# Kernel optimization log

Measured on AMD Instinct MI355X. Metric: run time of the kernel, lower is better.

## Reference

```python
import jax, jax.numpy as jnp
import numpy as np
import math

IN_CH = 256
OUT_CH = 256
N_JOINTS = 25
BATCH = 16384


def setup_inputs() -> dict:
    key = jax.random.key(0)
    kx, kw = jax.random.split(key)
    x = jax.random.normal(kx, (N_JOINTS, BATCH, IN_CH), dtype=jnp.float32)
    stdv = 1.0 / math.sqrt(OUT_CH)
    weight = jax.random.uniform(kw, (IN_CH, OUT_CH), dtype=jnp.float32,
                                minval=-stdv, maxval=stdv)
    return {"x": x, "weight": weight}


def reference(x, weight):
    # x: (N, B, D) -> attention over joints N per batch element
    xb = jnp.transpose(x, (1, 0, 2))            # (B, N, D)
    s3 = jnp.einsum('bnd,bmd->bnm', xb, xb)     # (B, N, N) self-similarity
    s = jax.nn.softmax(s3, axis=-1)
    out = jnp.einsum('bnm,bmd->bnd', s, xb)     # (B, N, D)
    out = out @ weight                           # (B, N, out_channels)
    return out
```

## Files before the change

### kernel.cpp

```cpp
#include <hip/hip_runtime.h>

#define GRID   1024
#define BLOCK  256
#define BATCH  16384
#define NJ     25
#define DEPTH  256
#define ITERS  (BATCH / GRID)

typedef short s16x8 __attribute__((ext_vector_type(8)));
typedef short s16x4 __attribute__((ext_vector_type(4)));
typedef float f32x4 __attribute__((ext_vector_type(4)));

__device__ __forceinline__ short f2bf(float f) {
  union { float f; unsigned u; } c; c.f = f;
  unsigned r = (c.u + 0x7FFFu + ((c.u >> 16) & 1u)) >> 16;
  return (short)r;
}

#define MFMA(a, b, c) __builtin_amdgcn_mfma_f32_16x16x32_bf16((a), (b), (c), 0, 0, 0)

__global__ __launch_bounds__(BLOCK, 2)
void geo_gcn_fused(const float* __restrict__ x,
                   const float* __restrict__ w,
                   float* __restrict__ out)
{
  __shared__ short As[2][32][72];
  __shared__ short Ps[32][40];
  __shared__ float S3[32][33];
  __shared__ short Yt[4][64][40];

  const int tid  = threadIdx.x;
  const int wv   = tid >> 6;
  const int lane = tid & 63;
  const int quad = lane >> 4;
  const int l16  = lane & 15;

  s16x8 wf[8][4];
  {
    const int ncol = wv * 64 + l16;
#pragma unroll
    for (int ks = 0; ks < 8; ++ks)
#pragma unroll
      for (int td = 0; td < 4; ++td) {
        const float* wp = w + (size_t)(ks * 32 + quad * 8) * DEPTH + ncol + td * 16;
#pragma unroll
        for (int j = 0; j < 8; ++j)
          wf[ks][td][j] = f2bf(wp[(size_t)j * DEPTH]);
      }
  }

  const int tm_s = wv >> 1;
  const int tn_s = wv & 1;

  const int srow = tid >> 3;
  const int sq   = tid & 7;

  for (int ib = 0; ib < ITERS; ++ib) {
    const int b = blockIdx.x + GRID * ib;

    f32x4 sacc = (f32x4){0.f, 0.f, 0.f, 0.f};
    f32x4 yacc[2][4];
#pragma unroll
    for (int i = 0; i < 2; ++i)
#pragma unroll
      for (int j = 0; j < 4; ++j) yacc[i][j] = (f32x4){0.f, 0.f, 0.f, 0.f};

    const float* xb = x + ((size_t)srow * BATCH + b) * DEPTH + sq * 8;

    {
      float4 c0, c1;
      if (srow < NJ) {
        c0 = *(const float4*)(xb + 0);
        c1 = *(const float4*)(xb + 4);
      } else { c0 = make_float4(0.f, 0.f, 0.f, 0.f); c1 = c0; }
      s16x8 h;
      h[0]=f2bf(c0.x); h[1]=f2bf(c0.y); h[2]=f2bf(c0.z); h[3]=f2bf(c0.w);
      h[4]=f2bf(c1.x); h[5]=f2bf(c1.y); h[6]=f2bf(c1.z); h[7]=f2bf(c1.w);
      *(s16x8*)&As[0][srow][sq * 8] = h;
    }
    __syncthreads();

#pragma unroll
    for (int kc = 0; kc < 4; ++kc) {
      float4 n0, n1;
      if (kc < 3) {
        if (srow < NJ) {
          n0 = *(const float4*)(xb + (kc + 1) * 64);
          n1 = *(const float4*)(xb + (kc + 1) * 64 + 4);
        } else { n0 = make_float4(0.f, 0.f, 0.f, 0.f); n1 = n0; }
      }
      const int buf = kc & 1;
#pragma unroll
      for (int s = 0; s < 2; ++s) {
        s16x8 a0 = *(const s16x8*)&As[buf][l16][s * 32 + quad * 8];
        s16x8 a1 = *(const s16x8*)&As[buf][16 + l16][s * 32 + quad * 8];
        sacc = MFMA(tm_s ? a1 : a0, tn_s ? a1 : a0, sacc);
        const int ks = kc * 2 + s;
#pragma unroll
        for (int td = 0; td < 4; ++td) {
          yacc[0][td] = MFMA(a0, wf[ks][td], yacc[0][td]);
          yacc[1][td] = MFMA(a1, wf[ks][td], yacc[1][td]);
        }
      }
      if (kc < 3) {
        s16x8 h;
        h[0]=f2bf(n0.x); h[1]=f2bf(n0.y); h[2]=f2bf(n0.z); h[3]=f2bf(n0.w);
        h[4]=f2bf(n1.x); h[5]=f2bf(n1.y); h[6]=f2bf(n1.z); h[7]=f2bf(n1.w);
        *(s16x8*)&As[1 - buf][srow][sq * 8] = h;
      }
      __syncthreads();
    }

#pragma unroll
    for (int r = 0; r < 4; ++r)
      S3[tm_s * 16 + quad * 4 + r][tn_s * 16 + l16] = sacc[r];
    __syncthreads();

    if (tid < 32) {
      const int row = tid;
      float mx = -3.0e38f;
      for (int j = 0; j < NJ; ++j) mx = fmaxf(mx, S3[row][j]);
      float sum = 0.f;
      for (int j = 0; j < NJ; ++j) sum += __expf(S3[row][j] - mx);
      const float rinv = 1.0f / sum;
      for (int j = 0; j < NJ; ++j) Ps[row][j] = f2bf(__expf(S3[row][j] - mx) * rinv);
      for (int j = NJ; j < 32; ++j) Ps[row][j] = 0;
    }
    __syncthreads();

#pragma unroll
    for (int tm = 0; tm < 2; ++tm)
#pragma unroll
      for (int td = 0; td < 4; ++td) {
        s16x4 hy;
#pragma unroll
        for (int r = 0; r < 4; ++r) hy[r] = f2bf(yacc[tm][td][r]);
        *(s16x4*)&Yt[wv][td * 16 + l16][tm * 16 + quad * 4] = hy;
      }

    s16x8 pf0 = *(const s16x8*)&Ps[l16][quad * 8];
    s16x8 pf1 = *(const s16x8*)&Ps[16 + l16][quad * 8];
    const f32x4 zero4 = (f32x4){0.f, 0.f, 0.f, 0.f};
    float* ob = out + (size_t)b * NJ * DEPTH + wv * 64 + l16;
#pragma unroll
    for (int td = 0; td < 4; ++td) {
      s16x8 yb = *(const s16x8*)&Yt[wv][td * 16 + l16][quad * 8];
      f32x4 o0 = MFMA(pf0, yb, zero4);
      f32x4 o1 = MFMA(pf1, yb, zero4);
#pragma unroll
      for (int r = 0; r < 4; ++r) {
        const int n0 = quad * 4 + r;
        ob[(size_t)n0 * DEPTH + td * 16] = o0[r];
        const int n1 = 16 + quad * 4 + r;
        if (n1 < NJ) ob[(size_t)n1 * DEPTH + td * 16] = o1[r];
      }
    }
  }
}

extern "C" void kernel_launch(void* const* d_in, const int* in_sizes, int n_in,
                              void* d_out, int out_size, void* d_ws, size_t ws_size,
                              hipStream_t stream) {
  (void)in_sizes; (void)n_in; (void)out_size; (void)d_ws; (void)ws_size;
  const float* x = (const float*)d_in[0];
  const float* w = (const float*)d_in[1];
  float* out = (float*)d_out;
  geo_gcn_fused<<<dim3(GRID), dim3(BLOCK), 0, stream>>>(x, w, out);
}
```

Before: 727.2 us.

## Use 8-wave blocks with whole-sample double-buffered prefetch and parallel softmax

Doubles the block to 512 threads (8 waves) and halves the grid. Each wave now owns 32 output columns, so it keeps half as many weight fragments in registers. Each block stages a full 25x256 bf16 sample in LDS and prefetches the next sample during the current iteration, which replaces the per-k-chunk loop and its repeated barriers. Softmax is spread over 256 threads using shuffle reductions instead of 32 serial threads. The tradeoffs are larger LDS use, only 4 of the 8 waves computing S, and prefetch registers that stay live across the whole iteration.

```diff
diff --git a/kernel.cpp b/kernel.cpp
--- a/kernel.cpp
+++ b/kernel.cpp
@@ -1,7 +1,7 @@
 #include <hip/hip_runtime.h>
 
-#define GRID   1024
-#define BLOCK  256
+#define GRID   512
+#define BLOCK  512
 #define BATCH  16384
 #define NJ     25
 #define DEPTH  256
@@ -19,15 +19,15 @@
 
 #define MFMA(a, b, c) __builtin_amdgcn_mfma_f32_16x16x32_bf16((a), (b), (c), 0, 0, 0)
 
-__global__ __launch_bounds__(BLOCK, 2)
+__global__ __launch_bounds__(BLOCK, 4)
 void geo_gcn_fused(const float* __restrict__ x,
                    const float* __restrict__ w,
                    float* __restrict__ out)
 {
-  __shared__ short As[2][32][72];
+  __shared__ short As[2][32][264];
   __shared__ short Ps[32][40];
   __shared__ float S3[32][33];
-  __shared__ short Yt[4][64][40];
+  __shared__ short Yt[8][32][40];
 
   const int tid  = threadIdx.x;
   const int wv   = tid >> 6;
@@ -35,13 +35,13 @@
   const int quad = lane >> 4;
   const int l16  = lane & 15;
 
-  s16x8 wf[8][4];
+  s16x8 wf[8][2];
   {
-    const int ncol = wv * 64 + l16;
+    const int ncol = wv * 32 + l16;
 #pragma unroll
     for (int ks = 0; ks < 8; ++ks)
 #pragma unroll
-      for (int td = 0; td < 4; ++td) {
+      for (int td = 0; td < 2; ++td) {
         const float* wp = w + (size_t)(ks * 32 + quad * 8) * DEPTH + ncol + td * 16;
 #pragma unroll
         for (int j = 0; j < 8; ++j)
@@ -49,89 +49,99 @@
       }
   }
 
-  const int tm_s = wv >> 1;
+  const int srow = tid >> 4;
+  const int sc   = tid & 15;
+  const int tm_s = (wv >> 1) & 1;
   const int tn_s = wv & 1;
 
-  const int srow = tid >> 3;
-  const int sq   = tid & 7;
+  const float* xrow = x + (size_t)srow * BATCH * DEPTH + sc * 16;
+
+  {
+    float4 c0 = make_float4(0.f, 0.f, 0.f, 0.f), c1 = c0, c2 = c0, c3 = c0;
+    if (srow < NJ) {
+      const float* xp = xrow + (size_t)blockIdx.x * DEPTH;
+      c0 = *(const float4*)(xp + 0);  c1 = *(const float4*)(xp + 4);
+      c2 = *(const float4*)(xp + 8);  c3 = *(const float4*)(xp + 12);
+    }
+    s16x8 h0, h1;
+    h0[0]=f2bf(c0.x); h0[1]=f2bf(c0.y); h0[2]=f2bf(c0.z); h0[3]=f2bf(c0.w);
+    h0[4]=f2bf(c1.x); h0[5]=f2bf(c1.y); h0[6]=f2bf(c1.z); h0[7]=f2bf(c1.w);
+    h1[0]=f2bf(c2.x); h1[1]=f2bf(c2.y); h1[2]=f2bf(c2.z); h1[3]=f2bf(c2.w);
+    h1[4]=f2bf(c3.x); h1[5]=f2bf(c3.y); h1[6]=f2bf(c3.z); h1[7]=f2bf(c3.w);
+    *(s16x8*)&As[0][srow][sc * 16]     = h0;
+    *(s16x8*)&As[0][srow][sc * 16 + 8] = h1;
+  }
+  __syncthreads();
 
   for (int ib = 0; ib < ITERS; ++ib) {
-    const int b = blockIdx.x + GRID * ib;
+    const int b   = blockIdx.x + GRID * ib;
+    const int buf = ib & 1;
+
+    float4 n0 = make_float4(0.f, 0.f, 0.f, 0.f), n1 = n0, n2 = n0, n3 = n0;
+    if ((ib + 1 < ITERS) && (srow < NJ)) {
+      const float* xp = xrow + (size_t)(b + GRID) * DEPTH;
+      n0 = *(const float4*)(xp + 0);  n1 = *(const float4*)(xp + 4);
+      n2 = *(const float4*)(xp + 8);  n3 = *(const float4*)(xp + 12);
+    }
 
     f32x4 sacc = (f32x4){0.f, 0.f, 0.f, 0.f};
-    f32x4 yacc[2][4];
+    f32x4 yacc[2][2];
 #pragma unroll
     for (int i = 0; i < 2; ++i)
 #pragma unroll
-      for (int j = 0; j < 4; ++j) yacc[i][j] = (f32x4){0.f, 0.f, 0.f, 0.f};
+      for (int j = 0; j < 2; ++j) yacc[i][j] = (f32x4){0.f, 0.f, 0.f, 0.f};
 
-    const float* xb = x + ((size_t)srow * BATCH + b) * DEPTH + sq * 8;
+#pragma unroll
+    for (int ks = 0; ks < 8; ++ks) {
+      s16x8 a0 = *(const s16x8*)&As[buf][l16][ks * 32 + quad * 8];
+      s16x8 a1 = *(const s16x8*)&As[buf][16 + l16][ks * 32 + quad * 8];
+      if (wv < 4) sacc = MFMA(tm_s ? a1 : a0, tn_s ? a1 : a0, sacc);
+      yacc[0][0] = MFMA(a0, wf[ks][0], yacc[0][0]);
+      yacc[0][1] = MFMA(a0, wf[ks][1], yacc[0][1]);
+      yacc[1][0] = MFMA(a1, wf[ks][0], yacc[1][0]);
+      yacc[1][1] = MFMA(a1, wf[ks][1], yacc[1][1]);
+    }
 
-    {
-      float4 c0, c1;
-      if (srow < NJ) {
-        c0 = *(const float4*)(xb + 0);
-        c1 = *(const float4*)(xb + 4);
-      } else { c0 = make_float4(0.f, 0.f, 0.f, 0.f); c1 = c0; }
-      s16x8 h;
-      h[0]=f2bf(c0.x); h[1]=f2bf(c0.y); h[2]=f2bf(c0.z); h[3]=f2bf(c0.w);
-      h[4]=f2bf(c1.x); h[5]=f2bf(c1.y); h[6]=f2bf(c1.z); h[7]=f2bf(c1.w);
-      *(s16x8*)&As[0][srow][sq * 8] = h;
+    if (wv < 4) {
+#pragma unroll
+      for (int r = 0; r < 4; ++r)
+        S3[tm_s * 16 + quad * 4 + r][tn_s * 16 + l16] = sacc[r];
     }
     __syncthreads();
 
+    if (tid < 256) {
+      const int row = tid >> 3, c8 = tid & 7;
+      float v[4]; float mx = -3.0e38f;
 #pragma unroll
-    for (int kc = 0; kc < 4; ++kc) {
-      float4 n0, n1;
-      if (kc < 3) {
-        if (srow < NJ) {
-          n0 = *(const float4*)(xb + (kc + 1) * 64);
-          n1 = *(const float4*)(xb + (kc + 1) * 64 + 4);
-        } else { n0 = make_float4(0.f, 0.f, 0.f, 0.f); n1 = n0; }
+      for (int i = 0; i < 4; ++i) {
+        const int j = c8 + 8 * i;
+        v[i] = (j < NJ) ? S3[row][j] : -3.0e38f;
+        mx = fmaxf(mx, v[i]);
       }
-      const int buf = kc & 1;
+      mx = fmaxf(mx, __shfl_xor(mx, 1));
+      mx = fmaxf(mx, __shfl_xor(mx, 2));
+      mx = fmaxf(mx, __shfl_xor(mx, 4));
+      float e[4]; float sum = 0.f;
 #pragma unroll
-      for (int s = 0; s < 2; ++s) {
-        s16x8 a0 = *(const s16x8*)&As[buf][l16][s * 32 + quad * 8];
-        s16x8 a1 = *(const s16x8*)&As[buf][16 + l16][s * 32 + quad * 8];
-        sacc = MFMA(tm_s ? a1 : a0, tn_s ? a1 : a0, sacc);
-        const int ks = kc * 2 + s;
+      for (int i = 0; i < 4; ++i) {
+        const int j = c8 + 8 * i;
+        e[i] = (j < NJ) ? __expf(v[i] - mx) : 0.f;
+        sum += e[i];
+      }
+      sum += __shfl_xor(sum, 1);
+      sum += __shfl_xor(sum, 2);
+      sum += __shfl_xor(sum, 4);
+      const float rinv = 1.0f / sum;
 #pragma unroll
-        for (int td = 0; td < 4; ++td) {
-          yacc[0][td] = MFMA(a0, wf[ks][td], yacc[0][td]);
-          yacc[1][td] = MFMA(a1, wf[ks][td], yacc[1][td]);
-        }
-      }
-      if (kc < 3) {
-        s16x8 h;
-        h[0]=f2bf(n0.x); h[1]=f2bf(n0.y); h[2]=f2bf(n0.z); h[3]=f2bf(n0.w);
-        h[4]=f2bf(n1.x); h[5]=f2bf(n1.y); h[6]=f2bf(n1.z); h[7]=f2bf(n1.w);
-        *(s16x8*)&As[1 - buf][srow][sq * 8] = h;
-      }
-      __syncthreads();
-    }
-
-#pragma unroll
-    for (int r = 0; r < 4; ++r)
-      S3[tm_s * 16 + quad * 4 + r][tn_s * 16 + l16] = sacc[r];
-    __syncthreads();
-
-    if (tid < 32) {
-      const int row = tid;
-      float mx = -3.0e38f;
-      for (int j = 0; j < NJ; ++j) mx = fmaxf(mx, S3[row][j]);
-      float sum = 0.f;
-      for (int j = 0; j < NJ; ++j) sum += __expf(S3[row][j] - mx);
-      const float rinv = 1.0f / sum;
-      for (int j = 0; j < NJ; ++j) Ps[row][j] = f2bf(__expf(S3[row][j] - mx) * rinv);
-      for (int j = NJ; j < 32; ++j) Ps[row][j] = 0;
+      for (int i = 0; i < 4; ++i)
+        Ps[row][c8 + 8 * i] = f2bf(e[i] * rinv);
     }
     __syncthreads();
 
 #pragma unroll
     for (int tm = 0; tm < 2; ++tm)
 #pragma unroll
-      for (int td = 0; td < 4; ++td) {
+      for (int td = 0; td < 2; ++td) {
         s16x4 hy;
 #pragma unroll
         for (int r = 0; r < 4; ++r) hy[r] = f2bf(yacc[tm][td][r]);
@@ -140,21 +150,31 @@
 
     s16x8 pf0 = *(const s16x8*)&Ps[l16][quad * 8];
     s16x8 pf1 = *(const s16x8*)&Ps[16 + l16][quad * 8];
-    const f32x4 zero4 = (f32x4){0.f, 0.f, 0.f, 0.f};
-    float* ob = out + (size_t)b * NJ * DEPTH + wv * 64 + l16;
+    const f32x4 z4 = (f32x4){0.f, 0.f, 0.f, 0.f};
+    float* ob = out + (size_t)b * NJ * DEPTH + wv * 32 + l16;
 #pragma unroll
-    for (int td = 0; td < 4; ++td) {
+    for (int td = 0; td < 2; ++td) {
       s16x8 yb = *(const s16x8*)&Yt[wv][td * 16 + l16][quad * 8];
-      f32x4 o0 = MFMA(pf0, yb, zero4);
-      f32x4 o1 = MFMA(pf1, yb, zero4);
+      f32x4 o0 = MFMA(pf0, yb, z4);
+      f32x4 o1 = MFMA(pf1, yb, z4);
 #pragma unroll
       for (int r = 0; r < 4; ++r) {
-        const int n0 = quad * 4 + r;
-        ob[(size_t)n0 * DEPTH + td * 16] = o0[r];
-        const int n1 = 16 + quad * 4 + r;
-        if (n1 < NJ) ob[(size_t)n1 * DEPTH + td * 16] = o1[r];
+        ob[(size_t)(quad * 4 + r) * DEPTH + td * 16] = o0[r];
+        const int nr = 16 + quad * 4 + r;
+        if (nr < NJ) ob[(size_t)nr * DEPTH + td * 16] = o1[r];
       }
     }
+
+    if (ib + 1 < ITERS) {
+      s16x8 h0, h1;
+      h0[0]=f2bf(n0.x); h0[1]=f2bf(n0.y); h0[2]=f2bf(n0.z); h0[3]=f2bf(n0.w);
+      h0[4]=f2bf(n1.x); h0[5]=f2bf(n1.y); h0[6]=f2bf(n1.z); h0[7]=f2bf(n1.w);
+      h1[0]=f2bf(n2.x); h1[1]=f2bf(n2.y); h1[2]=f2bf(n2.z); h1[3]=f2bf(n2.w);
+      h1[4]=f2bf(n3.x); h1[5]=f2bf(n3.y); h1[6]=f2bf(n3.z); h1[7]=f2bf(n3.w);
+      *(s16x8*)&As[1 - buf][srow][sc * 16]     = h0;
+      *(s16x8*)&As[1 - buf][srow][sc * 16 + 8] = h1;
+    }
+    __syncthreads();
   }
 }
 
```

New measurement: 793.5 us. +9.1%, slower.

## Assign one batch element per wavefront with register-resident softmax and LDS weights

Applied to the files above, without the earlier changes.

Each wavefront now processes a whole batch element on its own: it keeps the bf16 x fragments in registers, computes the 25x25 similarity with four MFMAs, and does the softmax with cross-lane shuffles. This removes the block-wide __syncthreads and the LDS staging for S3, Ps and Yt. The weight matrix moves from per-thread registers into a transposed bf16 LDS tile shared by 8 waves per block, and Y is repacked into MFMA operand layout with shuffles. The trade-off is about 132KB of LDS per block, which caps occupancy, and heavier register use from holding 16 x fragments per lane.

```diff
diff --git a/kernel.cpp b/kernel.cpp
--- a/kernel.cpp
+++ b/kernel.cpp
@@ -1,20 +1,25 @@
 #include <hip/hip_runtime.h>
 
-#define GRID   1024
-#define BLOCK  256
+#define GRID   256
+#define BLOCK  512
 #define BATCH  16384
 #define NJ     25
 #define DEPTH  256
-#define ITERS  (BATCH / GRID)
+#define WPB    8
+#define TOTW   (GRID * WPB)
+#define ELEMS  (BATCH / TOTW)
 
 typedef short s16x8 __attribute__((ext_vector_type(8)));
-typedef short s16x4 __attribute__((ext_vector_type(4)));
 typedef float f32x4 __attribute__((ext_vector_type(4)));
 
 __device__ __forceinline__ short f2bf(float f) {
   union { float f; unsigned u; } c; c.f = f;
   unsigned r = (c.u + 0x7FFFu + ((c.u >> 16) & 1u)) >> 16;
   return (short)r;
+}
+__device__ __forceinline__ unsigned pk2(float lo, float hi) {
+  return ((unsigned)(unsigned short)f2bf(hi) << 16) |
+         (unsigned)(unsigned short)f2bf(lo);
 }
 
 #define MFMA(a, b, c) __builtin_amdgcn_mfma_f32_16x16x32_bf16((a), (b), (c), 0, 0, 0)
@@ -24,135 +29,151 @@
                    const float* __restrict__ w,
                    float* __restrict__ out)
 {
-  __shared__ short As[2][32][72];
-  __shared__ short Ps[32][40];
-  __shared__ float S3[32][33];
-  __shared__ short Yt[4][64][40];
+  __shared__ short Wt[DEPTH][264];
 
   const int tid  = threadIdx.x;
   const int wv   = tid >> 6;
   const int lane = tid & 63;
-  const int quad = lane >> 4;
+  const int q    = lane >> 4;
   const int l16  = lane & 15;
 
-  s16x8 wf[8][4];
-  {
-    const int ncol = wv * 64 + l16;
+  for (int it = 0; it < 32; ++it) {
+    const int idx4 = tid + BLOCK * it;
+    const int k    = idx4 >> 6;
+    const int n4   = (idx4 & 63) << 2;
+    float4 wq = *(const float4*)(w + (size_t)k * DEPTH + n4);
+    Wt[n4 + 0][k] = f2bf(wq.x);
+    Wt[n4 + 1][k] = f2bf(wq.y);
+    Wt[n4 + 2][k] = f2bf(wq.z);
+    Wt[n4 + 3][k] = f2bf(wq.w);
+  }
+  __syncthreads();
+
+  const int gw = blockIdx.x * WPB + wv;
+  const float* xr0 = x + (size_t)l16 * BATCH * DEPTH + q * 8;
+  const float* xr1 = x + (size_t)(16 + l16) * BATCH * DEPTH + q * 8;
+  const bool  r1ok = (l16 < NJ - 16);
+  const int   sA   = ((q & 1) << 5) + l16;
+  const int   sB   = sA + 16;
+  const bool  lo32 = (lane < 32);
+  const f32x4 z4   = (f32x4){0.f, 0.f, 0.f, 0.f};
+  const s16x8 z8   = (s16x8){0, 0, 0, 0, 0, 0, 0, 0};
+
+  for (int i = 0; i < ELEMS; ++i) {
+    const int b = gw + TOTW * i;
+    const size_t boff = (size_t)b * DEPTH;
+
+    s16x8 af0[8], af1[8];
 #pragma unroll
-    for (int ks = 0; ks < 8; ++ks)
-#pragma unroll
-      for (int td = 0; td < 4; ++td) {
-        const float* wp = w + (size_t)(ks * 32 + quad * 8) * DEPTH + ncol + td * 16;
-#pragma unroll
-        for (int j = 0; j < 8; ++j)
-          wf[ks][td][j] = f2bf(wp[(size_t)j * DEPTH]);
-      }
-  }
-
-  const int tm_s = wv >> 1;
-  const int tn_s = wv & 1;
-
-  const int srow = tid >> 3;
-  const int sq   = tid & 7;
-
-  for (int ib = 0; ib < ITERS; ++ib) {
-    const int b = blockIdx.x + GRID * ib;
-
-    f32x4 sacc = (f32x4){0.f, 0.f, 0.f, 0.f};
-    f32x4 yacc[2][4];
-#pragma unroll
-    for (int i = 0; i < 2; ++i)
-#pragma unroll
-      for (int j = 0; j < 4; ++j) yacc[i][j] = (f32x4){0.f, 0.f, 0.f, 0.f};
-
-    const float* xb = x + ((size_t)srow * BATCH + b) * DEPTH + sq * 8;
-
-    {
-      float4 c0, c1;
-      if (srow < NJ) {
-        c0 = *(const float4*)(xb + 0);
-        c1 = *(const float4*)(xb + 4);
-      } else { c0 = make_float4(0.f, 0.f, 0.f, 0.f); c1 = c0; }
+    for (int ks = 0; ks < 8; ++ks) {
+      float4 c0 = *(const float4*)(xr0 + boff + ks * 32);
+      float4 c1 = *(const float4*)(xr0 + boff + ks * 32 + 4);
       s16x8 h;
       h[0]=f2bf(c0.x); h[1]=f2bf(c0.y); h[2]=f2bf(c0.z); h[3]=f2bf(c0.w);
       h[4]=f2bf(c1.x); h[5]=f2bf(c1.y); h[6]=f2bf(c1.z); h[7]=f2bf(c1.w);
-      *(s16x8*)&As[0][srow][sq * 8] = h;
+      af0[ks] = h;
+      s16x8 g = z8;
+      if (r1ok) {
+        float4 d0 = *(const float4*)(xr1 + boff + ks * 32);
+        float4 d1 = *(const float4*)(xr1 + boff + ks * 32 + 4);
+        g[0]=f2bf(d0.x); g[1]=f2bf(d0.y); g[2]=f2bf(d0.z); g[3]=f2bf(d0.w);
+        g[4]=f2bf(d1.x); g[5]=f2bf(d1.y); g[6]=f2bf(d1.z); g[7]=f2bf(d1.w);
+      }
+      af1[ks] = g;
     }
-    __syncthreads();
 
+    f32x4 s00 = z4, s01 = z4, s10 = z4, s11 = z4;
 #pragma unroll
-    for (int kc = 0; kc < 4; ++kc) {
-      float4 n0, n1;
-      if (kc < 3) {
-        if (srow < NJ) {
-          n0 = *(const float4*)(xb + (kc + 1) * 64);
-          n1 = *(const float4*)(xb + (kc + 1) * 64 + 4);
-        } else { n0 = make_float4(0.f, 0.f, 0.f, 0.f); n1 = n0; }
-      }
-      const int buf = kc & 1;
+    for (int ks = 0; ks < 8; ++ks) {
+      s00 = MFMA(af0[ks], af0[ks], s00);
+      s01 = MFMA(af0[ks], af1[ks], s01);
+      s10 = MFMA(af1[ks], af0[ks], s10);
+      s11 = MFMA(af1[ks], af1[ks], s11);
+    }
+
+    unsigned pd0[2][2], pd1[2][2];
+    {
+      float m0 = fmaxf(fmaxf(s00[0], s00[1]), fmaxf(s00[2], s00[3]));
+      float m1 = fmaxf(fmaxf(s01[0], s01[1]), fmaxf(s01[2], s01[3]));
 #pragma unroll
-      for (int s = 0; s < 2; ++s) {
-        s16x8 a0 = *(const s16x8*)&As[buf][l16][s * 32 + quad * 8];
-        s16x8 a1 = *(const s16x8*)&As[buf][16 + l16][s * 32 + quad * 8];
-        sacc = MFMA(tm_s ? a1 : a0, tn_s ? a1 : a0, sacc);
-        const int ks = kc * 2 + s;
-#pragma unroll
-        for (int td = 0; td < 4; ++td) {
-          yacc[0][td] = MFMA(a0, wf[ks][td], yacc[0][td]);
-          yacc[1][td] = MFMA(a1, wf[ks][td], yacc[1][td]);
+      for (int r = 0; r < 4; ++r) {
+        if (4 * q + r < 9) {
+          m0 = fmaxf(m0, s10[r]);
+          m1 = fmaxf(m1, s11[r]);
         }
       }
-      if (kc < 3) {
-        s16x8 h;
-        h[0]=f2bf(n0.x); h[1]=f2bf(n0.y); h[2]=f2bf(n0.z); h[3]=f2bf(n0.w);
-        h[4]=f2bf(n1.x); h[5]=f2bf(n1.y); h[6]=f2bf(n1.z); h[7]=f2bf(n1.w);
-        *(s16x8*)&As[1 - buf][srow][sq * 8] = h;
+      m0 = fmaxf(m0, __shfl_xor(m0, 16)); m0 = fmaxf(m0, __shfl_xor(m0, 32));
+      m1 = fmaxf(m1, __shfl_xor(m1, 16)); m1 = fmaxf(m1, __shfl_xor(m1, 32));
+      float e00[4], e01[4], e10[4], e11[4];
+      float t0 = 0.f, t1 = 0.f;
+#pragma unroll
+      for (int r = 0; r < 4; ++r) {
+        const bool v = (4 * q + r) < 9;
+        e00[r] = __expf(s00[r] - m0);
+        e10[r] = __expf(s01[r] - m1);
+        e01[r] = v ? __expf(s10[r] - m0) : 0.f;
+        e11[r] = v ? __expf(s11[r] - m1) : 0.f;
+        t0 += e00[r] + e01[r];
+        t1 += e10[r] + e11[r];
       }
-      __syncthreads();
+      t0 += __shfl_xor(t0, 16); t0 += __shfl_xor(t0, 32);
+      t1 += __shfl_xor(t1, 16); t1 += __shfl_xor(t1, 32);
+      const float i0 = 1.0f / t0, i1 = 1.0f / t1;
+      pd0[0][0] = pk2(e00[0] * i0, e00[1] * i0);
+      pd0[0][1] = pk2(e00[2] * i0, e00[3] * i0);
+      pd0[1][0] = pk2(e01[0] * i0, e01[1] * i0);
+      pd0[1][1] = pk2(e01[2] * i0, e01[3] * i0);
+      pd1[0][0] = pk2(e10[0] * i1, e10[1] * i1);
+      pd1[0][1] = pk2(e10[2] * i1, e10[3] * i1);
+      pd1[1][0] = pk2(e11[0] * i1, e11[1] * i1);
+      pd1[1][1] = pk2(e11[2] * i1, e11[3] * i1);
     }
 
+    s16x8 pf0, pf1;
+    {
+      union { unsigned u[4]; s16x8 v; } p0, p1;
+      int a, c;
+      a = __shfl((int)pd0[0][0], sA); c = __shfl((int)pd0[1][0], sA); p0.u[0] = lo32 ? a : c;
+      a = __shfl((int)pd0[0][1], sA); c = __shfl((int)pd0[1][1], sA); p0.u[1] = lo32 ? a : c;
+      a = __shfl((int)pd0[0][0], sB); c = __shfl((int)pd0[1][0], sB); p0.u[2] = lo32 ? a : c;
+      a = __shfl((int)pd0[0][1], sB); c = __shfl((int)pd0[1][1], sB); p0.u[3] = lo32 ? a : c;
+      a = __shfl((int)pd1[0][0], sA); c = __shfl((int)pd1[1][0], sA); p1.u[0] = lo32 ? a : c;
+      a = __shfl((int)pd1[0][1], sA); c = __shfl((int)pd1[1][1], sA); p1.u[1] = lo32 ? a : c;
+      a = __shfl((int)pd1[0][0], sB); c = __shfl((int)pd1[1][0], sB); p1.u[2] = lo32 ? a : c;
+      a = __shfl((int)pd1[0][1], sB); c = __shfl((int)pd1[1][1], sB); p1.u[3] = lo32 ? a : c;
+      pf0 = p0.v;
+      pf1 = p1.v;
+    }
+
+    float* ob = out + (size_t)b * NJ * DEPTH;
+#pragma unroll 2
+    for (int td = 0; td < 16; ++td) {
+      const short* wp = &Wt[16 * td + l16][q * 8];
+      f32x4 y0 = z4, y1 = z4;
 #pragma unroll
-    for (int r = 0; r < 4; ++r)
-      S3[tm_s * 16 + quad * 4 + r][tn_s * 16 + l16] = sacc[r];
-    __syncthreads();
-
-    if (tid < 32) {
-      const int row = tid;
-      float mx = -3.0e38f;
-      for (int j = 0; j < NJ; ++j) mx = fmaxf(mx, S3[row][j]);
-      float sum = 0.f;
-      for (int j = 0; j < NJ; ++j) sum += __expf(S3[row][j] - mx);
-      const float rinv = 1.0f / sum;
-      for (int j = 0; j < NJ; ++j) Ps[row][j] = f2bf(__expf(S3[row][j] - mx) * rinv);
-      for (int j = NJ; j < 32; ++j) Ps[row][j] = 0;
-    }
-    __syncthreads();
-
-#pragma unroll
-    for (int tm = 0; tm < 2; ++tm)
-#pragma unroll
-      for (int td = 0; td < 4; ++td) {
-        s16x4 hy;
-#pragma unroll
-        for (int r = 0; r < 4; ++r) hy[r] = f2bf(yacc[tm][td][r]);
-        *(s16x4*)&Yt[wv][td * 16 + l16][tm * 16 + quad * 4] = hy;
+      for (int ks = 0; ks < 8; ++ks) {
+        const s16x8 wb = *(const s16x8*)(wp + ks * 32);
+        y0 = MFMA(af0[ks], wb, y0);
+        y1 = MFMA(af1[ks], wb, y1);
       }
-
-    s16x8 pf0 = *(const s16x8*)&Ps[l16][quad * 8];
-    s16x8 pf1 = *(const s16x8*)&Ps[16 + l16][quad * 8];
-    const f32x4 zero4 = (f32x4){0.f, 0.f, 0.f, 0.f};
-    float* ob = out + (size_t)b * NJ * DEPTH + wv * 64 + l16;
-#pragma unroll
-    for (int td = 0; td < 4; ++td) {
-      s16x8 yb = *(const s16x8*)&Yt[wv][td * 16 + l16][quad * 8];
-      f32x4 o0 = MFMA(pf0, yb, zero4);
-      f32x4 o1 = MFMA(pf1, yb, zero4);
+      const unsigned a0 = pk2(y0[0], y0[1]), a1 = pk2(y0[2], y0[3]);
+      const unsigned b0 = pk2(y1[0], y1[1]), b1 = pk2(y1[2], y1[3]);
+      union { unsigned u[4]; s16x8 v; } yu;
+      {
+        int u0, u1;
+        u0 = __shfl((int)a0, sA); u1 = __shfl((int)b0, sA); yu.u[0] = lo32 ? u0 : u1;
+        u0 = __shfl((int)a1, sA); u1 = __shfl((int)b1, sA); yu.u[1] = lo32 ? u0 : u1;
+        u0 = __shfl((int)a0, sB); u1 = __shfl((int)b0, sB); yu.u[2] = lo32 ? u0 : u1;
+        u0 = __shfl((int)a1, sB); u1 = __shfl((int)b1, sB); yu.u[3] = lo32 ? u0 : u1;
+      }
+      f32x4 o0 = MFMA(pf0, yu.v, z4);
+      f32x4 o1 = MFMA(pf1, yu.v, z4);
+      float* op = ob + 16 * td + l16;
 #pragma unroll
       for (int r = 0; r < 4; ++r) {
-        const int n0 = quad * 4 + r;
-        ob[(size_t)n0 * DEPTH + td * 16] = o0[r];
-        const int n1 = 16 + quad * 4 + r;
-        if (n1 < NJ) ob[(size_t)n1 * DEPTH + td * 16] = o1[r];
+        op[(size_t)(4 * q + r) * DEPTH] = o0[r];
+        const int nr = 16 + 4 * q + r;
+        if (nr < NJ) op[(size_t)nr * DEPTH] = o1[r];
       }
     }
   }
```

Measured after the change: 722.2 us. No clear change (-0.7%).
